# Kernel tuning notes

Hardware: AMD Instinct MI355X
Metric: run time of the kernel (lower is better)

## Reference

```python
import jax, jax.numpy as jnp
import numpy as np

BLOCK_L = 32
STRIDE = 16
DIM = 128
N_DOWN = 5  # log2(BLOCK_L)


def setup_inputs() -> dict:
    key = jax.random.key(0)
    ks = jax.random.split(key, 4)
    B, H, S, D = 2, 16, 8192, DIM
    k = jax.random.normal(ks[0], (B, H, S, D), dtype=jnp.float32)
    pe = jax.random.normal(ks[1], (BLOCK_L, D), dtype=jnp.float32)
    # torch Linear weights [out, in]; down: Linear(2*dim, dim), scaled like default init
    w_down = jax.random.normal(ks[2], (N_DOWN, D, 2 * D), dtype=jnp.float32) / jnp.sqrt(2.0 * D)
    w_stop = jax.random.normal(ks[3], (D, D), dtype=jnp.float32) / jnp.sqrt(1.0 * D)
    return {"k": k, "pe": pe, "w_down": w_down, "w_stop": w_stop}


def reference(k, pe, w_down, w_stop):
    B, H, S, D = k.shape
    L = pe.shape[0]
    nb = (S - L) // STRIDE + 1  # number of sliding windows
    # unfold(-2, L, STRIDE).mT -> [B, H, nb, L, D]
    idx = STRIDE * jnp.arange(nb)[:, None] + jnp.arange(L)[None, :]  # [nb, L]
    x = k[:, :, idx, :] + pe  # broadcast pe over [B, H, nb]
    # prepend a zero block along the window axis
    x = jnp.concatenate([jnp.zeros_like(x[:, :, :1]), x], axis=2)  # [B, H, nb+1, L, D]
    # Phi: hierarchical pairwise merge, log2(L) stages
    for i in range(N_DOWN):
        Lc = x.shape[-2]
        x = x.reshape(*x.shape[:-2], Lc // 2, 2 * D)
        x = jax.nn.silu(jnp.einsum('...i,oi->...o', x, w_down[i]))
    out = jnp.einsum('...i,oi->...o', x, w_stop)  # [B, H, nb+1, 1, D]
    return out.squeeze(-2)
```

## Files before the change

kernel.cpp:

```cpp
#include <hip/hip_runtime.h>

#define BQ 2
#define HQ 16
#define SQ 8192
#define DQ 128
#define STR 16
#define NWIN 511
#define NBLK 512
#define WPB 8
#define NWG_PER_HEAD 64

typedef float f32x4 __attribute__((ext_vector_type(4)));
typedef short s16x8 __attribute__((ext_vector_type(8)));
typedef short s16x4 __attribute__((ext_vector_type(4)));

#define R_KIN 0u
#define R_S0  20480u
#define R_S1  0u
#define R_S2  20480u
#define R_S3  0u
#define R_S4  28672u

static __device__ __forceinline__ unsigned swz(unsigned b) {
    return b ^ (((b >> 9) & 7u) << 4);
}

static __device__ __forceinline__ short f2bf(float f) {
    __bf16 h = (__bf16)f;
    return __builtin_bit_cast(short, h);
}

static __device__ __forceinline__ float silu(float v) {
    return v * __builtin_amdgcn_rcpf(1.f + __expf(-v));
}

__global__ void prep_kernel(const float* __restrict__ wd,
                            const float* __restrict__ wstop,
                            const float* __restrict__ pe,
                            short* __restrict__ o,
                            float* __restrict__ bias,
                            float* __restrict__ out) {
    int blk = blockIdx.x;
    if (blk < 704) {
        int i = blk * 256 + threadIdx.x;
        if (i < 163840) {
            int s   = i >> 15;
            int r   = i & 32767;
            int ct  = r >> 12;
            int r2  = r & 4095;
            int kt  = r2 >> 9;
            int r3  = r2 & 511;
            int ln  = r3 >> 3;
            int e   = r3 & 7;
            int ch  = ct * 16 + (ln & 15);
            int k   = kt * 32 + (ln >> 4) * 8 + e;
            o[i] = f2bf(wd[((size_t)(s * 128 + ch)) * 256 + k]);
        } else if (i < 180224) {
            int j   = i - 163840;
            int ct  = j >> 11;
            int r2  = j & 2047;
            int kt  = r2 >> 9;
            int r3  = r2 & 511;
            int ln  = r3 >> 3;
            int e   = r3 & 7;
            int ch  = ct * 16 + (ln & 15);
            int k   = kt * 32 + (ln >> 4) * 8 + e;
            o[i] = f2bf(wstop[ch * 128 + k]);
        }
    } else if (blk < 712) {
        int oo = (blk - 704) * 256 + threadIdx.x;
        int j = oo >> 7;
        int c = oo & 127;
        const float* w  = wd + (size_t)c * 256;
        const float* p0 = pe + (2 * j) * DQ;
        const float* p1 = pe + (2 * j + 1) * DQ;
        float s = 0.f;
        #pragma unroll 4
        for (int i = 0; i < 128; ++i) s += w[i] * p0[i];
        #pragma unroll 4
        for (int i = 0; i < 128; ++i) s += w[i + 128] * p1[i];
        bias[oo] = s;
    } else {
        int i = (blk - 712) * 256 + threadIdx.x;
        int bh = i >> 7, d = i & 127;
        out[(size_t)bh * NBLK * DQ + d] = 0.f;
    }
}

__global__ __launch_bounds__(512, 6)
void fused_kernel(const float* __restrict__ kin,
                  const short* __restrict__ wdb,
                  const float* __restrict__ bias0,
                  float* __restrict__ out) {
    __shared__ __align__(16) unsigned char lds[53248];

    const int bh = blockIdx.x >> 6;
    const int w0 = (blockIdx.x & 63) * WPB;
    const int tid  = threadIdx.x;
    const int lane = tid & 63;
    const int ct   = tid >> 6;
    const int kl   = lane >> 4;
    const int nl   = lane & 15;

    const float* kb = kin + (size_t)bh * SQ * DQ;
    const short* wbase = wdb + ct * 4096 + lane * 8;

#define LOAD_KIN(cbase) {                                                      \
        _Pragma("unroll")                                                      \
        for (int it = 0; it < 3; ++it) {                                       \
            int task = tid + it * 512;                                         \
            if (task < 1280) {                                                 \
                int rr = task >> 4;                                            \
                int c8 = task & 15;                                            \
                int srow = STR * w0 + (cbase) + rr;                            \
                if (srow > SQ - 1) srow = SQ - 1;                              \
                const float* kp = kb + (size_t)srow * DQ + c8 * 8;             \
                f32x4 a0 = *(const f32x4*)kp;                                  \
                f32x4 a1 = *(const f32x4*)(kp + 4);                            \
                s16x8 v;                                                       \
                v[0]=f2bf(a0[0]); v[1]=f2bf(a0[1]); v[2]=f2bf(a0[2]); v[3]=f2bf(a0[3]); \
                v[4]=f2bf(a1[0]); v[5]=f2bf(a1[1]); v[6]=f2bf(a1[2]); v[7]=f2bf(a1[3]); \
                *(s16x8*)(lds + swz(R_KIN + (unsigned)((rr << 8) + (c8 << 4)))) = v; \
            }                                                                  \
        } }

#define K_HALF_AT(P, Q, off, accv) {                                           \
        s16x8 aa0 = *(const s16x8*)((P) + (off));                              \
        s16x8 aa1 = *(const s16x8*)((Q) + (off));                              \
        s16x8 aa2 = *(const s16x8*)((P) + (off) + 128);                        \
        s16x8 aa3 = *(const s16x8*)((Q) + (off) + 128);                        \
        accv = __builtin_amdgcn_mfma_f32_16x16x32_bf16(wfh[0], aa0, accv, 0, 0, 0); \
        accv = __builtin_amdgcn_mfma_f32_16x16x32_bf16(wfh[1], aa1, accv, 0, 0, 0); \
        accv = __builtin_amdgcn_mfma_f32_16x16x32_bf16(wfh[2], aa2, accv, 0, 0, 0); \
        accv = __builtin_amdgcn_mfma_f32_16x16x32_bf16(wfh[3], aa3, accv, 0, 0, 0); }

#define WRITE_ROW(region, d, accv) {                                           \
        s16x4 v;                                                               \
        v[0] = f2bf(silu((accv)[0])); v[1] = f2bf(silu((accv)[1]));            \
        v[2] = f2bf(silu((accv)[2])); v[3] = f2bf(silu((accv)[3]));            \
        *(s16x4*)(lds + swz((region) + ((unsigned)(d) << 8)                    \
                            + (unsigned)(ct * 32 + kl * 8))) = v; }

    const f32x4 bias = *(const f32x4*)(bias0 + nl * 128 + ct * 16 + kl * 4);

    LOAD_KIN(0);
    __syncthreads();

    #pragma unroll
    for (int c = 0; c < 2; ++c) {
        if (c) {
            __syncthreads();
            LOAD_KIN(64);
            __syncthreads();
        }
        f32x4 acc0 = bias, acc1 = bias, acc2 = bias, acc3 = bias;
        #pragma unroll
        for (int half = 0; half < 2; ++half) {
            s16x8 wfh[4];
            #pragma unroll
            for (int kt = 0; kt < 4; ++kt)
                wfh[kt] = *(const s16x8*)(wbase + (half * 4 + kt) * 512);
            unsigned pb = swz(R_KIN + ((unsigned)(2 * nl + half) << 8) + (unsigned)(kl << 4));
            const unsigned char* P = lds + pb;
            const unsigned char* Q = lds + (pb ^ 64u);
            K_HALF_AT(P, Q, 0,     acc0);
            K_HALF_AT(P, Q, 4096,  acc1);
            K_HALF_AT(P, Q, 8192,  acc2);
            K_HALF_AT(P, Q, 12288, acc3);
        }
        WRITE_ROW(R_S0, c * 64 + nl,      acc0);
        WRITE_ROW(R_S0, c * 64 + 16 + nl, acc1);
        WRITE_ROW(R_S0, c * 64 + 32 + nl, acc2);
        WRITE_ROW(R_S0, c * 64 + 48 + nl, acc3);
    }
    __syncthreads();

    {
        f32x4 acc0 = {}, acc1 = {}, acc2 = {}, acc3 = {};
        #pragma unroll
        for (int half = 0; half < 2; ++half) {
            s16x8 wfh[4];
            #pragma unroll
            for (int kt = 0; kt < 4; ++kt)
                wfh[kt] = *(const s16x8*)(wbase + 32768 + (half * 4 + kt) * 512);
            unsigned pb = swz(R_S0 + ((unsigned)(2 * nl + half) << 8) + (unsigned)(kl << 4));
            const unsigned char* P = lds + pb;
            const unsigned char* Q = lds + (pb ^ 64u);
            K_HALF_AT(P, Q, 0,     acc0);
            K_HALF_AT(P, Q, 8192,  acc1);
            K_HALF_AT(P, Q, 16384, acc2);
            K_HALF_AT(P, Q, 24576, acc3);
        }
        WRITE_ROW(R_S1, nl,      acc0);
        WRITE_ROW(R_S1, 16 + nl, acc1);
        WRITE_ROW(R_S1, 32 + nl, acc2);
        WRITE_ROW(R_S1, 48 + nl, acc3);
    }
    __syncthreads();

    {
        f32x4 acc0 = {}, acc1 = {};
        #pragma unroll
        for (int half = 0; half < 2; ++half) {
            s16x8 wfh[4];
            #pragma unroll
            for (int kt = 0; kt < 4; ++kt)
                wfh[kt] = *(const s16x8*)(wbase + 2 * 32768 + (half * 4 + kt) * 512);
            unsigned pb = swz(R_S1 + ((unsigned)(2 * nl + half) << 8) + (unsigned)(kl << 4));
            const unsigned char* P = lds + pb;
            const unsigned char* Q = lds + (pb ^ 64u);
            K_HALF_AT(P, Q, 0,    acc0);
            K_HALF_AT(P, Q, 8192, acc1);
        }
        WRITE_ROW(R_S2, nl,      acc0);
        WRITE_ROW(R_S2, 16 + nl, acc1);
    }
    __syncthreads();

    {
        f32x4 acc0 = {};
        #pragma unroll
        for (int half = 0; half < 2; ++half) {
            s16x8 wfh[4];
            #pragma unroll
            for (int kt = 0; kt < 4; ++kt)
                wfh[kt] = *(const s16x8*)(wbase + 3 * 32768 + (half * 4 + kt) * 512);
            unsigned pb = swz(R_S2 + ((unsigned)(2 * nl + half) << 8) + (unsigned)(kl << 4));
            const unsigned char* P = lds + pb;
            const unsigned char* Q = lds + (pb ^ 64u);
            K_HALF_AT(P, Q, 0, acc0);
        }
        WRITE_ROW(R_S3, nl, acc0);
    }
    __syncthreads();

    {
        int dc = (nl < 8) ? nl : 7;
        f32x4 acc0 = {};
        #pragma unroll
        for (int half = 0; half < 2; ++half) {
            s16x8 wfh[4];
            #pragma unroll
            for (int kt = 0; kt < 4; ++kt)
                wfh[kt] = *(const s16x8*)(wbase + 4 * 32768 + (half * 4 + kt) * 512);
            unsigned pb = swz(R_S3 + ((unsigned)(2 * dc + half) << 8) + (unsigned)(kl << 4));
            const unsigned char* P = lds + pb;
            const unsigned char* Q = lds + (pb ^ 64u);
            K_HALF_AT(P, Q, 0, acc0);
        }
        if (nl < 8) WRITE_ROW(R_S4, nl, acc0);
    }
    __syncthreads();

    {
        s16x8 wfh[4];
        #pragma unroll
        for (int kt = 0; kt < 4; ++kt)
            wfh[kt] = *(const s16x8*)(wdb + 163840 + ct * 2048 + kt * 512 + lane * 8);
        int dc = (nl < 8) ? nl : 7;
        f32x4 acc = {0.f, 0.f, 0.f, 0.f};
        unsigned pb = swz(R_S4 + ((unsigned)dc << 8) + (unsigned)(kl << 4));
        const unsigned char* P = lds + pb;
        const unsigned char* Q = lds + (pb ^ 64u);
        K_HALF_AT(P, Q, 0, acc);
        int w = w0 + nl;
        if (nl < 8 && w < NWIN) {
            *(f32x4*)(out + ((size_t)bh * NBLK + (w + 1)) * DQ + ct * 16 + kl * 4) = acc;
        }
    }
#undef K_HALF_AT
#undef WRITE_ROW
#undef LOAD_KIN
}

extern "C" void kernel_launch(void* const* d_in, const int* in_sizes, int n_in,
                              void* d_out, int out_size, void* d_ws, size_t ws_size,
                              hipStream_t stream) {
    const float* kin   = (const float*)d_in[0];
    const float* pe    = (const float*)d_in[1];
    const float* wdown = (const float*)d_in[2];
    const float* wstop = (const float*)d_in[3];
    float* out = (float*)d_out;
    short* wbf  = (short*)d_ws;
    float* bias = (float*)((char*)d_ws + 360448);

    prep_kernel<<<728, 256, 0, stream>>>(wdown, wstop, pe, wbf, bias, out);
    fused_kernel<<<BQ * HQ * NWG_PER_HEAD, 512, 0, stream>>>(kin, wbf, bias, out);
}
```

Measured before the change: 77.66 us.

## Prefetch next-stage weights and second input chunk into registers during compute

```diff
diff --git a/kernel.cpp b/kernel.cpp
--- a/kernel.cpp
+++ b/kernel.cpp
@@ -105,34 +105,19 @@
     const float* kb = kin + (size_t)bh * SQ * DQ;
     const short* wbase = wdb + ct * 4096 + lane * 8;
 
-#define LOAD_KIN(cbase) {                                                      \
-        _Pragma("unroll")                                                      \
-        for (int it = 0; it < 3; ++it) {                                       \
-            int task = tid + it * 512;                                         \
-            if (task < 1280) {                                                 \
-                int rr = task >> 4;                                            \
-                int c8 = task & 15;                                            \
-                int srow = STR * w0 + (cbase) + rr;                            \
-                if (srow > SQ - 1) srow = SQ - 1;                              \
-                const float* kp = kb + (size_t)srow * DQ + c8 * 8;             \
-                f32x4 a0 = *(const f32x4*)kp;                                  \
-                f32x4 a1 = *(const f32x4*)(kp + 4);                            \
-                s16x8 v;                                                       \
-                v[0]=f2bf(a0[0]); v[1]=f2bf(a0[1]); v[2]=f2bf(a0[2]); v[3]=f2bf(a0[3]); \
-                v[4]=f2bf(a1[0]); v[5]=f2bf(a1[1]); v[6]=f2bf(a1[2]); v[7]=f2bf(a1[3]); \
-                *(s16x8*)(lds + swz(R_KIN + (unsigned)((rr << 8) + (c8 << 4)))) = v; \
-            }                                                                  \
-        } }
-
-#define K_HALF_AT(P, Q, off, accv) {                                           \
+#define K_HALF4(W0, W1, W2, W3, P, Q, off, accv) {                             \
         s16x8 aa0 = *(const s16x8*)((P) + (off));                              \
         s16x8 aa1 = *(const s16x8*)((Q) + (off));                              \
         s16x8 aa2 = *(const s16x8*)((P) + (off) + 128);                        \
         s16x8 aa3 = *(const s16x8*)((Q) + (off) + 128);                        \
-        accv = __builtin_amdgcn_mfma_f32_16x16x32_bf16(wfh[0], aa0, accv, 0, 0, 0); \
-        accv = __builtin_amdgcn_mfma_f32_16x16x32_bf16(wfh[1], aa1, accv, 0, 0, 0); \
-        accv = __builtin_amdgcn_mfma_f32_16x16x32_bf16(wfh[2], aa2, accv, 0, 0, 0); \
-        accv = __builtin_amdgcn_mfma_f32_16x16x32_bf16(wfh[3], aa3, accv, 0, 0, 0); }
+        accv = __builtin_amdgcn_mfma_f32_16x16x32_bf16(W0, aa0, accv, 0, 0, 0); \
+        accv = __builtin_amdgcn_mfma_f32_16x16x32_bf16(W1, aa1, accv, 0, 0, 0); \
+        accv = __builtin_amdgcn_mfma_f32_16x16x32_bf16(W2, aa2, accv, 0, 0, 0); \
+        accv = __builtin_amdgcn_mfma_f32_16x16x32_bf16(W3, aa3, accv, 0, 0, 0); }
+
+#define K_FULL(P, Q, off, accv)                                                \
+        K_HALF4(wf[0], wf[1], wf[2], wf[3], P, Q, (off),       accv)           \
+        K_HALF4(wf[4], wf[5], wf[6], wf[7], P, Q, (off) + 256, accv)
 
 #define WRITE_ROW(region, d, accv) {                                           \
         s16x4 v;                                                               \
@@ -141,56 +126,111 @@
         *(s16x4*)(lds + swz((region) + ((unsigned)(d) << 8)                    \
                             + (unsigned)(ct * 32 + kl * 8))) = v; }
 
+#define LOAD_WF(stage_off) {                                                   \
+        _Pragma("unroll")                                                      \
+        for (int kt = 0; kt < 8; ++kt)                                         \
+            wf[kt] = *(const s16x8*)(wbase + (stage_off) + kt * 512); }
+
+    s16x8 wf[8];
+    LOAD_WF(0);
     const f32x4 bias = *(const f32x4*)(bias0 + nl * 128 + ct * 16 + kl * 4);
 
-    LOAD_KIN(0);
-    __syncthreads();
-
     #pragma unroll
-    for (int c = 0; c < 2; ++c) {
-        if (c) {
-            __syncthreads();
-            LOAD_KIN(64);
-            __syncthreads();
+    for (int it = 0; it < 3; ++it) {
+        int task = tid + it * 512;
+        if (task < 1280) {
+            int rr = task >> 4;
+            int c8 = task & 15;
+            int srow = STR * w0 + rr;
+            if (srow > SQ - 1) srow = SQ - 1;
+            const float* kp = kb + (size_t)srow * DQ + c8 * 8;
+            f32x4 a0 = *(const f32x4*)kp;
+            f32x4 a1 = *(const f32x4*)(kp + 4);
+            s16x8 v;
+            v[0]=f2bf(a0[0]); v[1]=f2bf(a0[1]); v[2]=f2bf(a0[2]); v[3]=f2bf(a0[3]);
+            v[4]=f2bf(a1[0]); v[5]=f2bf(a1[1]); v[6]=f2bf(a1[2]); v[7]=f2bf(a1[3]);
+            *(s16x8*)(lds + swz(R_KIN + (unsigned)((rr << 8) + (c8 << 4)))) = v;
         }
+    }
+    __syncthreads();
+
+    f32x4 pA0, pA1, pB0, pB1;
+    const int prow = tid >> 4, pc8 = tid & 15;
+    {
+        int sr = STR * w0 + 64 + prow;
+        if (sr > SQ - 1) sr = SQ - 1;
+        const float* kp = kb + (size_t)sr * DQ + pc8 * 8;
+        pA0 = *(const f32x4*)kp; pA1 = *(const f32x4*)(kp + 4);
+        sr = STR * w0 + 96 + prow;
+        if (sr > SQ - 1) sr = SQ - 1;
+        kp = kb + (size_t)sr * DQ + pc8 * 8;
+        pB0 = *(const f32x4*)kp; pB1 = *(const f32x4*)(kp + 4);
+    }
+
+    unsigned pb0 = swz(R_KIN + ((unsigned)(2 * nl) << 8) + (unsigned)(kl << 4));
+    const unsigned char* P0 = lds + pb0;
+    const unsigned char* Q0 = lds + (pb0 ^ 64u);
+
+    {
         f32x4 acc0 = bias, acc1 = bias, acc2 = bias, acc3 = bias;
-        #pragma unroll
-        for (int half = 0; half < 2; ++half) {
-            s16x8 wfh[4];
-            #pragma unroll
-            for (int kt = 0; kt < 4; ++kt)
-                wfh[kt] = *(const s16x8*)(wbase + (half * 4 + kt) * 512);
-            unsigned pb = swz(R_KIN + ((unsigned)(2 * nl + half) << 8) + (unsigned)(kl << 4));
-            const unsigned char* P = lds + pb;
-            const unsigned char* Q = lds + (pb ^ 64u);
-            K_HALF_AT(P, Q, 0,     acc0);
-            K_HALF_AT(P, Q, 4096,  acc1);
-            K_HALF_AT(P, Q, 8192,  acc2);
-            K_HALF_AT(P, Q, 12288, acc3);
+        K_FULL(P0, Q0, 0,     acc0);
+        K_FULL(P0, Q0, 4096,  acc1);
+        K_FULL(P0, Q0, 8192,  acc2);
+        K_FULL(P0, Q0, 12288, acc3);
+        WRITE_ROW(R_S0, nl,      acc0);
+        WRITE_ROW(R_S0, 16 + nl, acc1);
+        WRITE_ROW(R_S0, 32 + nl, acc2);
+        WRITE_ROW(R_S0, 48 + nl, acc3);
+    }
+    __syncthreads();
+
+    {
+        s16x8 v;
+        v[0]=f2bf(pA0[0]); v[1]=f2bf(pA0[1]); v[2]=f2bf(pA0[2]); v[3]=f2bf(pA0[3]);
+        v[4]=f2bf(pA1[0]); v[5]=f2bf(pA1[1]); v[6]=f2bf(pA1[2]); v[7]=f2bf(pA1[3]);
+        *(s16x8*)(lds + swz(R_KIN + (unsigned)((prow << 8) + (pc8 << 4)))) = v;
+        v[0]=f2bf(pB0[0]); v[1]=f2bf(pB0[1]); v[2]=f2bf(pB0[2]); v[3]=f2bf(pB0[3]);
+        v[4]=f2bf(pB1[0]); v[5]=f2bf(pB1[1]); v[6]=f2bf(pB1[2]); v[7]=f2bf(pB1[3]);
+        *(s16x8*)(lds + swz(R_KIN + (unsigned)(((32 + prow) << 8) + (pc8 << 4)))) = v;
+        if (tid < 256) {
+            int rr = 64 + (tid >> 4);
+            int c8 = tid & 15;
+            int sr = STR * w0 + 64 + rr;
+            if (sr > SQ - 1) sr = SQ - 1;
+            const float* kp = kb + (size_t)sr * DQ + c8 * 8;
+            f32x4 a0 = *(const f32x4*)kp;
+            f32x4 a1 = *(const f32x4*)(kp + 4);
+            v[0]=f2bf(a0[0]); v[1]=f2bf(a0[1]); v[2]=f2bf(a0[2]); v[3]=f2bf(a0[3]);
+            v[4]=f2bf(a1[0]); v[5]=f2bf(a1[1]); v[6]=f2bf(a1[2]); v[7]=f2bf(a1[3]);
+            *(s16x8*)(lds + swz(R_KIN + (unsigned)((rr << 8) + (c8 << 4)))) = v;
         }
-        WRITE_ROW(R_S0, c * 64 + nl,      acc0);
-        WRITE_ROW(R_S0, c * 64 + 16 + nl, acc1);
-        WRITE_ROW(R_S0, c * 64 + 32 + nl, acc2);
-        WRITE_ROW(R_S0, c * 64 + 48 + nl, acc3);
-    }
-    __syncthreads();
-
-    {
+    }
+    __syncthreads();
+
+    {
+        f32x4 acc0 = bias, acc1 = bias, acc2 = bias, acc3 = bias;
+        K_FULL(P0, Q0, 0,     acc0);
+        K_FULL(P0, Q0, 4096,  acc1);
+        K_FULL(P0, Q0, 8192,  acc2);
+        K_FULL(P0, Q0, 12288, acc3);
+        LOAD_WF(32768);
+        WRITE_ROW(R_S0, 64 + nl,  acc0);
+        WRITE_ROW(R_S0, 80 + nl,  acc1);
+        WRITE_ROW(R_S0, 96 + nl,  acc2);
+        WRITE_ROW(R_S0, 112 + nl, acc3);
+    }
+    __syncthreads();
+
+    {
+        unsigned pb = swz(R_S0 + ((unsigned)(2 * nl) << 8) + (unsigned)(kl << 4));
+        const unsigned char* P = lds + pb;
+        const unsigned char* Q = lds + (pb ^ 64u);
         f32x4 acc0 = {}, acc1 = {}, acc2 = {}, acc3 = {};
-        #pragma unroll
-        for (int half = 0; half < 2; ++half) {
-            s16x8 wfh[4];
-            #pragma unroll
-            for (int kt = 0; kt < 4; ++kt)
-                wfh[kt] = *(const s16x8*)(wbase + 32768 + (half * 4 + kt) * 512);
-            unsigned pb = swz(R_S0 + ((unsigned)(2 * nl + half) << 8) + (unsigned)(kl << 4));
-            const unsigned char* P = lds + pb;
-            const unsigned char* Q = lds + (pb ^ 64u);
-            K_HALF_AT(P, Q, 0,     acc0);
-            K_HALF_AT(P, Q, 8192,  acc1);
-            K_HALF_AT(P, Q, 16384, acc2);
-            K_HALF_AT(P, Q, 24576, acc3);
-        }
+        K_FULL(P, Q, 0,     acc0);
+        K_FULL(P, Q, 8192,  acc1);
+        K_FULL(P, Q, 16384, acc2);
+        K_FULL(P, Q, 24576, acc3);
+        LOAD_WF(2 * 32768);
         WRITE_ROW(R_S1, nl,      acc0);
         WRITE_ROW(R_S1, 16 + nl, acc1);
         WRITE_ROW(R_S1, 32 + nl, acc2);
@@ -199,78 +239,59 @@
     __syncthreads();
 
     {
+        unsigned pb = swz(R_S1 + ((unsigned)(2 * nl) << 8) + (unsigned)(kl << 4));
+        const unsigned char* P = lds + pb;
+        const unsigned char* Q = lds + (pb ^ 64u);
         f32x4 acc0 = {}, acc1 = {};
-        #pragma unroll
-        for (int half = 0; half < 2; ++half) {
-            s16x8 wfh[4];
-            #pragma unroll
-            for (int kt = 0; kt < 4; ++kt)
-                wfh[kt] = *(const s16x8*)(wbase + 2 * 32768 + (half * 4 + kt) * 512);
-            unsigned pb = swz(R_S1 + ((unsigned)(2 * nl + half) << 8) + (unsigned)(kl << 4));
-            const unsigned char* P = lds + pb;
-            const unsigned char* Q = lds + (pb ^ 64u);
-            K_HALF_AT(P, Q, 0,    acc0);
-            K_HALF_AT(P, Q, 8192, acc1);
-        }
+        K_FULL(P, Q, 0,    acc0);
+        K_FULL(P, Q, 8192, acc1);
+        LOAD_WF(3 * 32768);
         WRITE_ROW(R_S2, nl,      acc0);
         WRITE_ROW(R_S2, 16 + nl, acc1);
     }
     __syncthreads();
 
     {
+        unsigned pb = swz(R_S2 + ((unsigned)(2 * nl) << 8) + (unsigned)(kl << 4));
+        const unsigned char* P = lds + pb;
+        const unsigned char* Q = lds + (pb ^ 64u);
         f32x4 acc0 = {};
-        #pragma unroll
-        for (int half = 0; half < 2; ++half) {
-            s16x8 wfh[4];
-            #pragma unroll
-            for (int kt = 0; kt < 4; ++kt)
-                wfh[kt] = *(const s16x8*)(wbase + 3 * 32768 + (half * 4 + kt) * 512);
-            unsigned pb = swz(R_S2 + ((unsigned)(2 * nl + half) << 8) + (unsigned)(kl << 4));
-            const unsigned char* P = lds + pb;
-            const unsigned char* Q = lds + (pb ^ 64u);
-            K_HALF_AT(P, Q, 0, acc0);
-        }
+        K_FULL(P, Q, 0, acc0);
+        LOAD_WF(4 * 32768);
         WRITE_ROW(R_S3, nl, acc0);
     }
     __syncthreads();
 
     {
         int dc = (nl < 8) ? nl : 7;
+        unsigned pb = swz(R_S3 + ((unsigned)(2 * dc) << 8) + (unsigned)(kl << 4));
+        const unsigned char* P = lds + pb;
+        const unsigned char* Q = lds + (pb ^ 64u);
         f32x4 acc0 = {};
-        #pragma unroll
-        for (int half = 0; half < 2; ++half) {
-            s16x8 wfh[4];
-            #pragma unroll
-            for (int kt = 0; kt < 4; ++kt)
-                wfh[kt] = *(const s16x8*)(wbase + 4 * 32768 + (half * 4 + kt) * 512);
-            unsigned pb = swz(R_S3 + ((unsigned)(2 * dc + half) << 8) + (unsigned)(kl << 4));
-            const unsigned char* P = lds + pb;
-            const unsigned char* Q = lds + (pb ^ 64u);
-            K_HALF_AT(P, Q, 0, acc0);
-        }
-        if (nl < 8) WRITE_ROW(R_S4, nl, acc0);
-    }
-    __syncthreads();
-
-    {
-        s16x8 wfh[4];
+        K_FULL(P, Q, 0, acc0);
         #pragma unroll
         for (int kt = 0; kt < 4; ++kt)
-            wfh[kt] = *(const s16x8*)(wdb + 163840 + ct * 2048 + kt * 512 + lane * 8);
+            wf[kt] = *(const s16x8*)(wdb + 163840 + ct * 2048 + kt * 512 + lane * 8);
+        if (nl < 8) WRITE_ROW(R_S4, nl, acc0);
+    }
+    __syncthreads();
+
+    {
         int dc = (nl < 8) ? nl : 7;
+        unsigned pb = swz(R_S4 + ((unsigned)dc << 8) + (unsigned)(kl << 4));
+        const unsigned char* P = lds + pb;
+        const unsigned char* Q = lds + (pb ^ 64u);
         f32x4 acc = {0.f, 0.f, 0.f, 0.f};
-        unsigned pb = swz(R_S4 + ((unsigned)dc << 8) + (unsigned)(kl << 4));
-        const unsigned char* P = lds + pb;
-        const unsigned char* Q = lds + (pb ^ 64u);
-        K_HALF_AT(P, Q, 0, acc);
+        K_HALF4(wf[0], wf[1], wf[2], wf[3], P, Q, 0, acc);
         int w = w0 + nl;
         if (nl < 8 && w < NWIN) {
             *(f32x4*)(out + ((size_t)bh * NBLK + (w + 1)) * DQ + ct * 16 + kl * 4) = acc;
         }
     }
-#undef K_HALF_AT
+#undef K_HALF4
+#undef K_FULL
 #undef WRITE_ROW
-#undef LOAD_KIN
+#undef LOAD_WF
 }
 
 extern "C" void kernel_launch(void* const* d_in, const int* in_sizes, int n_in,
```

After: 77.20 us. No clear change (-0.6%).
